# Performance work log

Measured on AMD Instinct MI355X. Metric: run time of the kernel, lower is better.

## Reference

```python
import jax, jax.numpy as jnp
import numpy as np

B, R, C = 2, 64, 256
PH = PW = 7
KMAX = 8            # max pool-kernel size per axis given roi size bounds (kernel<=7 here)
HW = [160, 80, 40, 20]   # FPN level spatial sizes for a 640px image, strides 4/8/16/32
STRIDES = [4.0, 8.0, 16.0, 32.0]
TOP = 224.0         # config.top_pyramid_roi_size
HIDDEN = 2048
NCLS = 20
SCALE = float(np.round(np.sqrt(C), 2))  # np.round(sqrt(inner_dim),2) in SelfAttention


def setup_inputs() -> dict:
    key = jax.random.key(0)
    ks = jax.random.split(key, 32)
    U = lambda k, s, lo, hi: jax.random.uniform(k, s, minval=lo, maxval=hi)
    x1 = U(ks[0], (B, R), 0.0, 260.0)
    y1 = U(ks[1], (B, R), 0.0, 260.0)
    w = U(ks[2], (B, R), 16.0, 360.0)
    h = U(ks[3], (B, R), 16.0, 360.0)
    rois = jnp.stack([x1, y1, jnp.minimum(x1 + w, 639.0), jnp.minimum(y1 + h, 639.0)], -1)
    N = lambda k, s, sc: (sc * jax.random.normal(k, s)).astype(jnp.float32)
    inp = {'rois': rois}
    for i in range(4):
        inp[f'fm{i}'] = N(ks[4 + i], (B, C, HW[i], HW[i]), 1.0)
    inp['wq'] = N(ks[8], (C, C), 0.02);  inp['bq'] = jnp.zeros((C,), jnp.float32)
    inp['wk'] = N(ks[9], (C, C), 0.02);  inp['bk'] = jnp.zeros((C,), jnp.float32)
    inp['wv'] = N(ks[10], (C, C), 0.02); inp['bv'] = jnp.zeros((C,), jnp.float32)
    inp['wo'] = N(ks[11], (C, C), 0.02); inp['bo'] = jnp.zeros((C,), jnp.float32)
    inp['w1'] = N(ks[12], (C * PH * PW, HIDDEN), 0.02); inp['b1'] = jnp.zeros((HIDDEN,), jnp.float32)
    inp['w2'] = N(ks[13], (HIDDEN, HIDDEN), 0.02);       inp['b2'] = jnp.zeros((HIDDEN,), jnp.float32)
    inp['wreg'] = N(ks[14], (HIDDEN, 4 * (NCLS + 1)), 0.02); inp['breg'] = jnp.zeros((4 * (NCLS + 1),), jnp.float32)
    inp['wcls'] = N(ks[15], (HIDDEN, NCLS + 1), 0.02);       inp['bcls'] = jnp.zeros((NCLS + 1,), jnp.float32)
    return inp


def _forward(rois, fm0, fm1, fm2, fm3, wq, bq, wk, bk, wv, bv, wo, bo,
             w1, b1, w2, b2, wreg, breg, wcls, bcls):
    Hmax = HW[0]
    pad = lambda fm: jnp.pad(fm, ((0, 0), (0, 0), (0, Hmax - fm.shape[-2]), (0, Hmax - fm.shape[-1])))
    feats = jnp.stack([pad(fm0), pad(fm1), pad(fm2), pad(fm3)])  # [4,B,C,Hmax,Hmax]
    heights = jnp.array(HW, jnp.int32)
    strides = jnp.array(STRIDES, jnp.float32)

    r = rois.reshape(-1, 4)                 # [N,4] xyxy in pixels
    Nroi = r.shape[0]
    bidx = jnp.repeat(jnp.arange(B, dtype=jnp.int32), R)
    size = jnp.sqrt((r[:, 2] - r[:, 0]) * (r[:, 3] - r[:, 1]))
    # int() truncates toward zero, then clamp(0,3) -- matches torch
    lvl = jnp.clip((3.0 + jnp.log(size / TOP)).astype(jnp.int32), 0, 3)
    s = strides[lvl]
    x1 = (r[:, 0] / s).astype(jnp.int32); y1 = (r[:, 1] / s).astype(jnp.int32)
    x2 = (r[:, 2] / s).astype(jnp.int32); y2 = (r[:, 3] / s).astype(jnp.int32)
    Hl = heights[lvl]                        # per-roi level map size (square maps)

    def expand(lo, hi, cap, pool):
        # replicate the symmetric while-loop expansion until span >= pool
        for _ in range(pool):
            need = (hi - lo + 1) < pool
            lo = jnp.where(need, jnp.maximum(lo - 1, 0), lo)
            hi = jnp.where(need, jnp.minimum(hi + 1, cap - 1), hi)
        return lo, hi

    y1, y2 = expand(y1, y2, Hl, PH)
    x1, x2 = expand(x1, x2, Hl, PW)
    rh = y2 - y1 + 1; rw = x2 - x1 + 1
    kh = (rh + PH - 1) // PH; sh = rh // PH   # ceil / floor kernel & stride
    kw = (rw + PW - 1) // PW; sw = rw // PW

    ar_p = jnp.arange(PH); ar_k = jnp.arange(KMAX)

    def pool_one(l, b, yy, xx, kh_, kw_, sh_, sw_):
        rows = jnp.clip(yy + ar_p[:, None] * sh_ + ar_k[None, :], 0, Hmax - 1)  # [PH,K]
        cols = jnp.clip(xx + ar_p[:, None] * sw_ + ar_k[None, :], 0, Hmax - 1)  # [PW,K]
        patch = feats[l, b][:, rows[:, :, None, None], cols[None, None, :, :]]  # [C,PH,K,PW,K]
        m = (ar_k < kh_)[:, None, None] & (ar_k < kw_)[None, None, :]           # [K,1,K] -> bcast
        patch = jnp.where(m, patch, -jnp.inf)
        return patch.max(axis=(2, 4))                                           # [C,PH,PW]

    pooled = jax.vmap(pool_one)(lvl, bidx, y1, x1, kh, kw, sh, sw)  # [N,C,PH,PW]

    # SelfAttention over the PH*PW spatial tokens of each ROI
    L = PH * PW
    tok = pooled.reshape(Nroi, C, L).transpose(0, 2, 1)            # [N,L,C]
    q = tok @ wq + bq
    k = tok @ wk + bk
    v = tok @ wv + bv
    att = jax.nn.softmax(jnp.einsum('nlc,nmc->nlm', q, k) / SCALE, axis=-1)
    ctx = jnp.einsum('nlm,nmc->nlc', att, v) @ wo + bo             # [N,L,C]
    x = pooled.reshape(Nroi, C, L) + ctx.transpose(0, 2, 1)        # residual add
    x = x.reshape(Nroi, C * L)

    h1 = jax.nn.relu(x @ w1 + b1)
    h2 = jax.nn.relu(h1 @ w2 + b2)
    bbox_reg = h2 @ wreg + breg                                    # [N, 4*(NCLS+1)]
    bbox_classes = jax.nn.softmax(h2 @ wcls + bcls, axis=-1)       # [N, NCLS+1]
    return bbox_reg, bbox_classes


def reference(rois, fm0, fm1, fm2, fm3, wq, bq, wk, bk, wv, bv, wo, bo,
              w1, b1, w2, b2, wreg, breg, wcls, bcls):
    return _forward(rois, fm0, fm1, fm2, fm3, wq, bq, wk, bk, wv, bv, wo, bo,
                    w1, b1, w2, b2, wreg, breg, wcls, bcls)
```

## Files before the change

kernel.cpp:

```cpp
#include <hip/hip_runtime.h>
#include <hip/hip_bf16.h>
#include <stdint.h>

typedef __attribute__((ext_vector_type(8))) short bf16x8;
typedef __attribute__((ext_vector_type(4))) float f32x4;

__device__ __forceinline__ float blo(unsigned u){ union{float f;unsigned x;}v; v.x = u<<16; return v.f; }
__device__ __forceinline__ float bhi(unsigned u){ union{float f;unsigned x;}v; v.x = u & 0xFFFF0000u; return v.f; }
__device__ __forceinline__ unsigned short f2bf(float f){
  union{float f;unsigned x;}v; v.f=f; unsigned x=v.x;
  return (unsigned short)((x + 0x7fffu + ((x>>16)&1u)) >> 16);
}
__device__ __forceinline__ unsigned cvtpk(float lo, float hi){
  unsigned r;
  asm("v_cvt_pk_bf16_f32 %0, %1, %2" : "=v"(r) : "v"(lo), "v"(hi));
  return r;
}

__global__ __launch_bounds__(256) void pool_pack_kernel(
    const float* __restrict__ rois,
    const float* __restrict__ fm0, const float* __restrict__ fm1,
    const float* __restrict__ fm2, const float* __restrict__ fm3,
    float* __restrict__ pooled, unsigned short* __restrict__ tok,
    const float* __restrict__ wreg, const float* __restrict__ wcls, float* __restrict__ wT)
{
  int bx = blockIdx.x;
  int tid = threadIdx.x;
  if (bx >= 896){
    int c = bx - 896;
    if (c < 84){
      for (int k = tid; k < 2048; k += 256) wT[(size_t)c*2048 + k] = wreg[(size_t)k*84 + c];
    } else {
      int cc = c - 84;
      for (int k = tid; k < 2048; k += 256) wT[(size_t)c*2048 + k] = wcls[(size_t)k*21 + cc];
    }
    return;
  }
  int n = bx / 7;
  int ph = bx - n*7;
  int c = tid;
  const float* r = rois + n*4;
  int b = n >> 6;
  float rx1=r[0], ry1=r[1], rx2=r[2], ry2=r[3];
  float size = sqrtf((rx2-rx1)*(ry2-ry1));
  int lvl = (int)(3.0f + logf(size/224.0f));
  if (lvl < 0) lvl = 0; if (lvl > 3) lvl = 3;
  const float strides_[4] = {4.f,8.f,16.f,32.f};
  const int hw_[4] = {160,80,40,20};
  float s = strides_[lvl]; int Hl = hw_[lvl];
  int x1 = (int)(rx1/s), y1 = (int)(ry1/s), x2 = (int)(rx2/s), y2 = (int)(ry2/s);
  #pragma unroll
  for (int it=0; it<7; ++it){
    bool need = (y2-y1+1) < 7;
    if (need){ y1 = (y1-1 > 0) ? y1-1 : 0; y2 = (y2+1 < Hl-1) ? y2+1 : Hl-1; }
  }
  #pragma unroll
  for (int it=0; it<7; ++it){
    bool need = (x2-x1+1) < 7;
    if (need){ x1 = (x1-1 > 0) ? x1-1 : 0; x2 = (x2+1 < Hl-1) ? x2+1 : Hl-1; }
  }
  int rh = y2-y1+1, rw = x2-x1+1;
  int kh = (rh+6)/7, sh = rh/7, kw = (rw+6)/7, sw2 = rw/7;
  const float* fm = (lvl==0)?fm0:(lvl==1)?fm1:(lvl==2)?fm2:fm3;
  const float* fp = fm + ((size_t)(b*256 + c))*(size_t)(Hl*Hl);
  int r0 = y1 + ph*sh;
  for (int pw=0; pw<7; ++pw){
    int c0 = x1 + pw*sw2;
    float m = -3.4e38f;
    for (int i=0;i<kh;++i){
      const float* rp = fp + (size_t)(r0+i)*Hl + c0;
      for (int j=0;j<kw;++j) m = fmaxf(m, rp[j]);
    }
    int l = ph*7+pw;
    pooled[((size_t)n*256 + c)*49 + l] = m;
    tok[((size_t)n*49 + l)*256 + c] = f2bf(m);
  }
}

template<int EPI, bool XCDR>
__global__ __launch_bounds__(256) void gemm_kernel(
    const unsigned short* __restrict__ A,
    const float* __restrict__ B0, const float* __restrict__ B1, const float* __restrict__ B2,
    const float* __restrict__ bias0, const float* __restrict__ bias1, const float* __restrict__ bias2,
    unsigned short* __restrict__ o0, unsigned short* __restrict__ o1, unsigned short* __restrict__ o2,
    float* __restrict__ outf, const float* __restrict__ pooled,
    int M, int Nper, int K, int nM, int nN, int kChunk)
{
  __shared__ __align__(16) unsigned short Bs[2][2048];
  int bid = blockIdx.x;
  if constexpr (XCDR){
    int pe = gridDim.x >> 3;
    bid = (bid & 7)*pe + (bid >> 3);
  }
  int per = nM*nN;
  int kc  = bid / per;
  int rem = bid - kc*per;
  int bm = rem % nM, bn = rem / nM;
  int m0 = bm*64, n0 = bn*64;
  int mat = n0 / Nper;
  int col0 = n0 - mat*Nper;
  const float* Bp    = (mat==0)?B0:(mat==1)?B1:B2;
  const float* biasp = (mat==0)?bias0:(mat==1)?bias1:bias2;
  unsigned short* outp = (mat==0)?o0:(mat==1)?o1:o2;
  int k0 = kc*kChunk;
  int nMacro = kChunk >> 7;
  int tid = threadIdx.x, lane = tid & 63, wave = tid >> 6;
  int wm = wave & 1, wn = wave >> 1;
  int g = lane >> 4, c = lane & 15;

  f32x4 acc[2][2];
  #pragma unroll
  for (int i=0;i<2;++i)
    #pragma unroll
    for (int j=0;j<2;++j){ acc[i][j][0]=0.f; acc[i][j][1]=0.f; acc[i][j][2]=0.f; acc[i][j][3]=0.f; }

  int brow = tid >> 3, bcg = tid & 7;
  int bw_idx = brow*64 + ((bcg*8) ^ ((brow>>3)<<4));
  const float* Bbase = Bp + (size_t)brow*Nper + col0 + bcg*8;
  int rb0 = g*512 + (((wn*2  )^g)*16 + c);
  int rb1 = g*512 + (((wn*2+1)^g)*16 + c);
  const unsigned short* Ap0 = A + (size_t)(m0 + wm*32 +      c)*K + g*8;
  const unsigned short* Ap1 = A + (size_t)(m0 + wm*32 + 16 + c)*K + g*8;

  auto writeB = [&](int buf, const float4& bx, const float4& by){
    uint4 w;
    w.x = cvtpk(bx.x,bx.y); w.y = cvtpk(bx.z,bx.w);
    w.z = cvtpk(by.x,by.y); w.w = cvtpk(by.z,by.w);
    *(uint4*)&Bs[buf][bw_idx] = w;
  };
  auto readFrags = [&](int buf, bf16x8& r0, bf16x8& r1){
    union { unsigned short s[8]; bf16x8 v; } u0, u1;
    const unsigned short* bsp = &Bs[buf][0];
    #pragma unroll
    for (int j=0;j<8;++j){ u0.s[j] = bsp[rb0 + j*64]; u1.s[j] = bsp[rb1 + j*64]; }
    r0 = u0.v; r1 = u1.v;
  };
  auto mfma4 = [&](const bf16x8& f0, const bf16x8& f1, const bf16x8& q0, const bf16x8& q1){
    acc[0][0] = __builtin_amdgcn_mfma_f32_16x16x32_bf16(f0,q0,acc[0][0],0,0,0);
    acc[0][1] = __builtin_amdgcn_mfma_f32_16x16x32_bf16(f0,q1,acc[0][1],0,0,0);
    acc[1][0] = __builtin_amdgcn_mfma_f32_16x16x32_bf16(f1,q0,acc[1][0],0,0,0);
    acc[1][1] = __builtin_amdgcn_mfma_f32_16x16x32_bf16(f1,q1,acc[1][1],0,0,0);
  };

  for (int mi = 0; mi < nMacro; ++mi){
    int kk = k0 + (mi << 7);
    uint4 a0x = *(const uint4*)(Ap0+kk),    a0y = *(const uint4*)(Ap1+kk);
    uint4 a1x = *(const uint4*)(Ap0+kk+32), a1y = *(const uint4*)(Ap1+kk+32);
    uint4 a2x = *(const uint4*)(Ap0+kk+64), a2y = *(const uint4*)(Ap1+kk+64);
    uint4 a3x = *(const uint4*)(Ap0+kk+96), a3y = *(const uint4*)(Ap1+kk+96);
    const float* p0 = Bbase + (size_t)kk*Nper;
    const float* p1 = p0 + (size_t)32*Nper;
    const float* p2 = p0 + (size_t)64*Nper;
    const float* p3 = p0 + (size_t)96*Nper;
    float4 b0a = *(const float4*)p0, b0b = *(const float4*)(p0+4);
    float4 b1a = *(const float4*)p1, b1b = *(const float4*)(p1+4);
    float4 b2a = *(const float4*)p2, b2b = *(const float4*)(p2+4);
    float4 b3a = *(const float4*)p3, b3b = *(const float4*)(p3+4);

    writeB(0, b0a, b0b);
    __syncthreads();

    bf16x8 q0,q1;
    readFrags(0,q0,q1);
    writeB(1,b1a,b1b);
    mfma4(*(const bf16x8*)&a0x, *(const bf16x8*)&a0y, q0,q1);
    __syncthreads();

    readFrags(1,q0,q1);
    writeB(0,b2a,b2b);
    mfma4(*(const bf16x8*)&a1x, *(const bf16x8*)&a1y, q0,q1);
    __syncthreads();

    readFrags(0,q0,q1);
    writeB(1,b3a,b3b);
    mfma4(*(const bf16x8*)&a2x, *(const bf16x8*)&a2y, q0,q1);
    __syncthreads();

    readFrags(1,q0,q1);
    mfma4(*(const bf16x8*)&a3x, *(const bf16x8*)&a3y, q0,q1);
  }

  int rq = g << 2, cl = c;
  #pragma unroll
  for (int mr=0;mr<2;++mr){
    #pragma unroll
    for (int nc=0;nc<2;++nc){
      int rowb = m0 + wm*32 + mr*16 + rq;
      int colM = col0 + wn*32 + nc*16 + cl;
      #pragma unroll
      for (int r2=0;r2<4;++r2){
        float v = acc[mr][nc][r2];
        int rr = rowb + r2;
        if constexpr (EPI==0){
          v += biasp[colM];
          outp[(size_t)rr*Nper + colM] = f2bf(v);
        } else if constexpr (EPI==1){
          v += biasp[colM];
          int nn = rr/49, l = rr - nn*49;
          v += pooled[((size_t)nn*256 + colM)*49 + l];
          outp[(size_t)nn*12544 + colM*49 + l] = f2bf(v);
        } else {
          outf[(size_t)kc*M*Nper + (size_t)rr*Nper + colM] = v;
        }
      }
    }
  }
}

__global__ __launch_bounds__(256) void reduce1_kernel(
    const float* __restrict__ part, const float* __restrict__ b1,
    unsigned short* __restrict__ h1, int nPart)
{
  int i = blockIdx.x*256 + threadIdx.x;
  float4 s = ((const float4*)part)[i];
  for (int kc = 1; kc < nPart; ++kc){
    float4 p = ((const float4*)part)[(size_t)kc*65536 + i];
    s.x += p.x; s.y += p.y; s.z += p.z; s.w += p.w;
  }
  float4 bb = *(const float4*)(b1 + ((i<<2) & 2047));
  s.x = fmaxf(s.x+bb.x,0.f); s.y = fmaxf(s.y+bb.y,0.f);
  s.z = fmaxf(s.z+bb.z,0.f); s.w = fmaxf(s.w+bb.w,0.f);
  uint2 w;
  w.x = cvtpk(s.x, s.y); w.y = cvtpk(s.z, s.w);
  *(uint2*)&h1[(size_t)i<<2] = w;
}

__global__ __launch_bounds__(256) void reduce2_kernel(
    const float* __restrict__ part, float* __restrict__ h2f, int nPart)
{
  int i = blockIdx.x*256 + threadIdx.x;
  float4 s = ((const float4*)part)[i];
  for (int kc = 1; kc < nPart; ++kc){
    float4 p = ((const float4*)part)[(size_t)kc*65536 + i];
    s.x += p.x; s.y += p.y; s.z += p.z; s.w += p.w;
  }
  ((float4*)h2f)[i] = s;
}

__global__ __launch_bounds__(256) void attn_kernel(
    const unsigned short* __restrict__ Q, const unsigned short* __restrict__ Km,
    const unsigned short* __restrict__ V, unsigned short* __restrict__ ctx)
{
  int n = blockIdx.x, half = blockIdx.y, tid = threadIdx.x;
  int r0 = half*25, rcnt = half ? 24 : 25;
  __shared__ __align__(16) unsigned short qs[25*256];
  __shared__ __align__(16) unsigned short ks[49*260];
  __shared__ float S[25*49];
  const uint4* qg = (const uint4*)(Q + ((size_t)n*49 + r0)*256);
  for (int i = tid; i < rcnt*32; i += 256) ((uint4*)qs)[i] = qg[i];
  const uint2* kg = (const uint2*)(Km + (size_t)n*49*256);
  for (int i = tid; i < 49*64; i += 256){
    int j = i >> 6, s = i & 63;
    *(uint2*)(ks + j*260 + s*4) = kg[i];
  }
  __syncthreads();
  for (int p = tid; p < rcnt*49; p += 256){
    int i = p/49, j = p - i*49;
    const uint2* qr = (const uint2*)(qs + i*256);
    const uint2* kr = (const uint2*)(ks + j*260);
    float sum = 0.f;
    #pragma unroll 8
    for (int c4 = 0; c4 < 64; ++c4){
      uint2 qv = qr[c4], kv = kr[c4];
      sum += blo(qv.x)*blo(kv.x) + bhi(qv.x)*bhi(kv.x);
      sum += blo(qv.y)*blo(kv.y) + bhi(qv.y)*bhi(kv.y);
    }
    S[p] = sum * (1.0f/16.0f);
  }
  __syncthreads();
  const uint2* vg = (const uint2*)(V + (size_t)n*49*256);
  for (int i = tid; i < 49*64; i += 256){
    int j = i >> 6, s = i & 63;
    *(uint2*)(ks + j*260 + s*4) = vg[i];
  }
  if (tid < rcnt){
    float* row = S + tid*49;
    float mx = row[0];
    for (int j=1;j<49;++j) mx = fmaxf(mx,row[j]);
    float sm = 0.f;
    for (int j=0;j<49;++j){ float e = expf(row[j]-mx); row[j]=e; sm+=e; }
    float inv = 1.0f/sm;
    for (int j=0;j<49;++j) row[j] *= inv;
  }
  __syncthreads();
  for (int idx = tid; idx < rcnt*64; idx += 256){
    int i = idx >> 6, cp4 = idx & 63;
    const float* att = S + i*49;
    float s0=0.f, s1=0.f, s2=0.f, s3=0.f;
    #pragma unroll 7
    for (int j=0;j<49;++j){
      uint2 v = *(const uint2*)(ks + j*260 + cp4*4);
      float a = att[j];
      s0 += a*blo(v.x); s1 += a*bhi(v.x);
      s2 += a*blo(v.y); s3 += a*bhi(v.y);
    }
    uint2 outw;
    outw.x = (unsigned)f2bf(s0) | ((unsigned)f2bf(s1) << 16);
    outw.y = (unsigned)f2bf(s2) | ((unsigned)f2bf(s3) << 16);
    *(uint2*)&ctx[((size_t)n*49 + r0 + i)*256 + cp4*4] = outw;
  }
}

__global__ __launch_bounds__(256) void heads_dot(
    const float* __restrict__ h2f, const float* __restrict__ b2,
    const float* __restrict__ wT,
    const float* __restrict__ breg, const float* __restrict__ bcls,
    float* __restrict__ out, float* __restrict__ logits)
{
  int gw = (blockIdx.x*256 + threadIdx.x) >> 6;
  int lane = threadIdx.x & 63;
  int m = gw / 105, c = gw - m*105;
  const float4* hp = (const float4*)(h2f + (size_t)m*2048);
  const float4* bp = (const float4*)b2;
  const float4* wp = (const float4*)(wT + (size_t)c*2048);
  float sum = 0.f;
  #pragma unroll
  for (int i=0;i<8;++i){
    float4 a = hp[i*64 + lane];
    float4 bb = bp[i*64 + lane];
    float4 w = wp[i*64 + lane];
    sum += fmaxf(a.x+bb.x,0.f)*w.x + fmaxf(a.y+bb.y,0.f)*w.y
         + fmaxf(a.z+bb.z,0.f)*w.z + fmaxf(a.w+bb.w,0.f)*w.w;
  }
  #pragma unroll
  for (int off=32; off; off>>=1) sum += __shfl_down(sum, off, 64);
  if (lane == 0){
    if (c < 84) out[(size_t)m*84 + c] = sum + breg[c];
    else        logits[(size_t)m*21 + (c-84)] = sum + bcls[c-84];
  }
}

__global__ __launch_bounds__(128) void cls_softmax(
    const float* __restrict__ logits, float* __restrict__ out)
{
  int m = threadIdx.x;
  const float* lg = logits + (size_t)m*21;
  float mx = lg[0];
  #pragma unroll
  for (int j=1;j<21;++j) mx = fmaxf(mx, lg[j]);
  float sm = 0.f;
  float e[21];
  #pragma unroll
  for (int j=0;j<21;++j){ e[j] = expf(lg[j]-mx); sm += e[j]; }
  float inv = 1.0f/sm;
  #pragma unroll
  for (int j=0;j<21;++j) out[10752 + (size_t)m*21 + j] = e[j]*inv;
}

extern "C" void kernel_launch(void* const* d_in, const int* in_sizes, int n_in,
                              void* d_out, int out_size, void* d_ws, size_t ws_size,
                              hipStream_t stream)
{
  (void)in_sizes; (void)n_in; (void)out_size; (void)ws_size;
  const float* rois = (const float*)d_in[0];
  const float* fm0  = (const float*)d_in[1];
  const float* fm1  = (const float*)d_in[2];
  const float* fm2  = (const float*)d_in[3];
  const float* fm3  = (const float*)d_in[4];
  const float* wq   = (const float*)d_in[5];
  const float* bq   = (const float*)d_in[6];
  const float* wk   = (const float*)d_in[7];
  const float* bk   = (const float*)d_in[8];
  const float* wv   = (const float*)d_in[9];
  const float* bv   = (const float*)d_in[10];
  const float* wo   = (const float*)d_in[11];
  const float* bo   = (const float*)d_in[12];
  const float* w1   = (const float*)d_in[13];
  const float* b1   = (const float*)d_in[14];
  const float* w2   = (const float*)d_in[15];
  const float* b2   = (const float*)d_in[16];
  const float* wreg = (const float*)d_in[17];
  const float* breg = (const float*)d_in[18];
  const float* wcls = (const float*)d_in[19];
  const float* bcls = (const float*)d_in[20];
  float* out = (float*)d_out;

  char* ws = (char*)d_ws;
  float*          pooled = (float*)(ws + 0);
  unsigned short* tok    = (unsigned short*)(ws + 6422528);
  unsigned short* Qb     = (unsigned short*)(ws + 9633792);
  unsigned short* Kb     = (unsigned short*)(ws + 12845056);
  unsigned short* Vb     = (unsigned short*)(ws + 16056320);
  unsigned short* ctx    = (unsigned short*)(ws + 19267584);
  unsigned short* xb     = (unsigned short*)(ws + 22478848);
  float*          h2f    = (float*)(ws + 25690112);
  unsigned short* h1     = (unsigned short*)(ws + 26738688);
  float*          wT     = (float*)(ws + 27787264);
  float*          logits = (float*)(ws + 28647424);
  float*          h1part = (float*)(ws + 0);
  float*          h2part = (float*)(ws + 0);

  pool_pack_kernel<<<1001,256,0,stream>>>(rois, fm0, fm1, fm2, fm3, pooled, tok,
                                          wreg, wcls, wT);

  gemm_kernel<0,false><<<1176,256,0,stream>>>(tok, wq,wk,wv, bq,bk,bv,
                                              Qb,Kb,Vb, nullptr, nullptr,
                                              6272,256,256, 98,12, 256);

  attn_kernel<<<dim3(128,2),256,0,stream>>>(Qb, Kb, Vb, ctx);

  gemm_kernel<1,false><<<392,256,0,stream>>>(ctx, wo,wo,wo, bo,bo,bo,
                                             xb,xb,xb, nullptr, pooled,
                                             6272,256,256, 98,4, 256);

  gemm_kernel<2,true><<<896,256,0,stream>>>(xb, w1,w1,w1, nullptr,nullptr,nullptr,
                                            nullptr,nullptr,nullptr, h1part, nullptr,
                                            128,2048,12544, 2,32, 896);
  reduce1_kernel<<<256,256,0,stream>>>(h1part, b1, h1, 14);

  gemm_kernel<2,true><<<1024,256,0,stream>>>(h1, w2,w2,w2, nullptr,nullptr,nullptr,
                                             nullptr,nullptr,nullptr, h2part, nullptr,
                                             128,2048,2048, 2,32, 128);
  reduce2_kernel<<<256,256,0,stream>>>(h2part, h2f, 16);

  heads_dot<<<3360,256,0,stream>>>(h2f, b2, wT, breg, bcls, out, logits);
  cls_softmax<<<1,128,0,stream>>>(logits, out);
}
```

Measured before the change: 187.9 us.

## Stage fp32 weight tiles into LDS via direct global-to-LDS loads

The GEMM's B (weight) operand is now copied straight from global memory into an fp32 LDS double buffer with global_load_lds, rather than loaded into registers, converted to bf16 and written to LDS. Conversion to bf16 happens after the LDS read, just before the MFMAs. The loop now steps 32 k-values per iteration with a prefetch of the next tile, replacing the 128-wide macro step. The aim is to cut register pressure and VGPR-to-LDS store traffic. In exchange it doubles LDS footprint, adds conversion work on every fragment read, and puts a barrier on every 32-k step, losing the multi-step register prefetch of A and B.

```diff
diff --git a/kernel.cpp b/kernel.cpp
--- a/kernel.cpp
+++ b/kernel.cpp
@@ -15,6 +15,11 @@
   unsigned r;
   asm("v_cvt_pk_bf16_f32 %0, %1, %2" : "=v"(r) : "v"(lo), "v"(hi));
   return r;
+}
+__device__ __forceinline__ void gll16(const float* g, float* l){
+  __builtin_amdgcn_global_load_lds(
+      (const __attribute__((address_space(1))) unsigned int*)g,
+      (__attribute__((address_space(3))) unsigned int*)l, 16, 0, 0);
 }
 
 __global__ __launch_bounds__(256) void pool_pack_kernel(
@@ -86,7 +91,7 @@
     float* __restrict__ outf, const float* __restrict__ pooled,
     int M, int Nper, int K, int nM, int nN, int kChunk)
 {
-  __shared__ __align__(16) unsigned short Bs[2][2048];
+  __shared__ __align__(16) float Bs[2][32][64];
   int bid = blockIdx.x;
   if constexpr (XCDR){
     int pe = gridDim.x >> 3;
@@ -102,8 +107,7 @@
   const float* Bp    = (mat==0)?B0:(mat==1)?B1:B2;
   const float* biasp = (mat==0)?bias0:(mat==1)?bias1:bias2;
   unsigned short* outp = (mat==0)?o0:(mat==1)?o1:o2;
-  int k0 = kc*kChunk;
-  int nMacro = kChunk >> 7;
+  int k0 = kc*kChunk, k1 = k0 + kChunk;
   int tid = threadIdx.x, lane = tid & 63, wave = tid >> 6;
   int wm = wave & 1, wn = wave >> 1;
   int g = lane >> 4, c = lane & 15;
@@ -114,70 +118,38 @@
     #pragma unroll
     for (int j=0;j<2;++j){ acc[i][j][0]=0.f; acc[i][j][1]=0.f; acc[i][j][2]=0.f; acc[i][j][3]=0.f; }
 
-  int brow = tid >> 3, bcg = tid & 7;
-  int bw_idx = brow*64 + ((bcg*8) ^ ((brow>>3)<<4));
-  const float* Bbase = Bp + (size_t)brow*Nper + col0 + bcg*8;
-  int rb0 = g*512 + (((wn*2  )^g)*16 + c);
-  int rb1 = g*512 + (((wn*2+1)^g)*16 + c);
+  const float* Bg = Bp + (size_t)(wave*8 + (lane>>4))*Nper + col0 + (lane&15)*4;
   const unsigned short* Ap0 = A + (size_t)(m0 + wm*32 +      c)*K + g*8;
   const unsigned short* Ap1 = A + (size_t)(m0 + wm*32 + 16 + c)*K + g*8;
 
-  auto writeB = [&](int buf, const float4& bx, const float4& by){
-    uint4 w;
-    w.x = cvtpk(bx.x,bx.y); w.y = cvtpk(bx.z,bx.w);
-    w.z = cvtpk(by.x,by.y); w.w = cvtpk(by.z,by.w);
-    *(uint4*)&Bs[buf][bw_idx] = w;
+  auto stage = [&](int buf, int kk){
+    gll16(Bg + (size_t)kk*Nper,     &Bs[buf][wave*8    ][0]);
+    gll16(Bg + (size_t)(kk+4)*Nper, &Bs[buf][wave*8 + 4][0]);
   };
-  auto readFrags = [&](int buf, bf16x8& r0, bf16x8& r1){
-    union { unsigned short s[8]; bf16x8 v; } u0, u1;
-    const unsigned short* bsp = &Bs[buf][0];
+
+  stage(0, k0);
+  int buf = 0;
+  for (int kk = k0; kk < k1; kk += 32){
+    __syncthreads();
+    if (kk + 32 < k1) stage(buf^1, kk+32);
+    uint4 a0 = *(const uint4*)(Ap0 + kk);
+    uint4 a1 = *(const uint4*)(Ap1 + kk);
+    const float* fb = &Bs[buf][g*8][wn*32 + c];
+    float q0f[8], q1f[8];
     #pragma unroll
-    for (int j=0;j<8;++j){ u0.s[j] = bsp[rb0 + j*64]; u1.s[j] = bsp[rb1 + j*64]; }
-    r0 = u0.v; r1 = u1.v;
-  };
-  auto mfma4 = [&](const bf16x8& f0, const bf16x8& f1, const bf16x8& q0, const bf16x8& q1){
-    acc[0][0] = __builtin_amdgcn_mfma_f32_16x16x32_bf16(f0,q0,acc[0][0],0,0,0);
-    acc[0][1] = __builtin_amdgcn_mfma_f32_16x16x32_bf16(f0,q1,acc[0][1],0,0,0);
-    acc[1][0] = __builtin_amdgcn_mfma_f32_16x16x32_bf16(f1,q0,acc[1][0],0,0,0);
-    acc[1][1] = __builtin_amdgcn_mfma_f32_16x16x32_bf16(f1,q1,acc[1][1],0,0,0);
-  };
-
-  for (int mi = 0; mi < nMacro; ++mi){
-    int kk = k0 + (mi << 7);
-    uint4 a0x = *(const uint4*)(Ap0+kk),    a0y = *(const uint4*)(Ap1+kk);
-    uint4 a1x = *(const uint4*)(Ap0+kk+32), a1y = *(const uint4*)(Ap1+kk+32);
-    uint4 a2x = *(const uint4*)(Ap0+kk+64), a2y = *(const uint4*)(Ap1+kk+64);
-    uint4 a3x = *(const uint4*)(Ap0+kk+96), a3y = *(const uint4*)(Ap1+kk+96);
-    const float* p0 = Bbase + (size_t)kk*Nper;
-    const float* p1 = p0 + (size_t)32*Nper;
-    const float* p2 = p0 + (size_t)64*Nper;
-    const float* p3 = p0 + (size_t)96*Nper;
-    float4 b0a = *(const float4*)p0, b0b = *(const float4*)(p0+4);
-    float4 b1a = *(const float4*)p1, b1b = *(const float4*)(p1+4);
-    float4 b2a = *(const float4*)p2, b2b = *(const float4*)(p2+4);
-    float4 b3a = *(const float4*)p3, b3b = *(const float4*)(p3+4);
-
-    writeB(0, b0a, b0b);
-    __syncthreads();
-
-    bf16x8 q0,q1;
-    readFrags(0,q0,q1);
-    writeB(1,b1a,b1b);
-    mfma4(*(const bf16x8*)&a0x, *(const bf16x8*)&a0y, q0,q1);
-    __syncthreads();
-
-    readFrags(1,q0,q1);
-    writeB(0,b2a,b2b);
-    mfma4(*(const bf16x8*)&a1x, *(const bf16x8*)&a1y, q0,q1);
-    __syncthreads();
-
-    readFrags(0,q0,q1);
-    writeB(1,b3a,b3b);
-    mfma4(*(const bf16x8*)&a2x, *(const bf16x8*)&a2y, q0,q1);
-    __syncthreads();
-
-    readFrags(1,q0,q1);
-    mfma4(*(const bf16x8*)&a3x, *(const bf16x8*)&a3y, q0,q1);
+    for (int j=0;j<8;++j){ q0f[j] = fb[j*64]; q1f[j] = fb[j*64 + 16]; }
+    union { unsigned u[4]; bf16x8 v; } q0u, q1u;
+    q0u.u[0]=cvtpk(q0f[0],q0f[1]); q0u.u[1]=cvtpk(q0f[2],q0f[3]);
+    q0u.u[2]=cvtpk(q0f[4],q0f[5]); q0u.u[3]=cvtpk(q0f[6],q0f[7]);
+    q1u.u[0]=cvtpk(q1f[0],q1f[1]); q1u.u[1]=cvtpk(q1f[2],q1f[3]);
+    q1u.u[2]=cvtpk(q1f[4],q1f[5]); q1u.u[3]=cvtpk(q1f[6],q1f[7]);
+    bf16x8 f0 = *(const bf16x8*)&a0;
+    bf16x8 f1 = *(const bf16x8*)&a1;
+    acc[0][0] = __builtin_amdgcn_mfma_f32_16x16x32_bf16(f0,q0u.v,acc[0][0],0,0,0);
+    acc[0][1] = __builtin_amdgcn_mfma_f32_16x16x32_bf16(f0,q1u.v,acc[0][1],0,0,0);
+    acc[1][0] = __builtin_amdgcn_mfma_f32_16x16x32_bf16(f1,q0u.v,acc[1][0],0,0,0);
+    acc[1][1] = __builtin_amdgcn_mfma_f32_16x16x32_bf16(f1,q1u.v,acc[1][1],0,0,0);
+    buf ^= 1;
   }
 
   int rq = g << 2, cl = c;
```

Result: no change. 184.8 us (-1.6%).

## Add LDS-async fc kernel with gathered w1 rows and token-major pooled layout

Applied to the files above, without the earlier changes.

Replaces the generic split-K GEMM for the two big FC layers with a dedicated fc_kernel. It streams fp32 weight rows into LDS through global_load_lds with a 4-deep buffer ring and explicit vmcnt waits, then converts to bf16 at fragment read. The activation x is now stored token-major (l*256+c), and w1 rows are gathered with a permuted index so the math still matches the channel-major flatten. The pooled buffer also moves to token-major to simplify the residual epilogue. The w1 GEMM is split into more K chunks (28 instead of 14), which raises parallelism at the cost of a larger partial-sum reduction.

```diff
diff --git a/kernel.cpp b/kernel.cpp
--- a/kernel.cpp
+++ b/kernel.cpp
@@ -15,6 +15,11 @@
   unsigned r;
   asm("v_cvt_pk_bf16_f32 %0, %1, %2" : "=v"(r) : "v"(lo), "v"(hi));
   return r;
+}
+__device__ __forceinline__ void gll16(const float* g, float* l){
+  __builtin_amdgcn_global_load_lds(
+      (const __attribute__((address_space(1))) unsigned int*)g,
+      (__attribute__((address_space(3))) unsigned int*)l, 16, 0, 0);
 }
 
 __global__ __launch_bounds__(256) void pool_pack_kernel(
@@ -72,26 +77,117 @@
       for (int j=0;j<kw;++j) m = fmaxf(m, rp[j]);
     }
     int l = ph*7+pw;
-    pooled[((size_t)n*256 + c)*49 + l] = m;
+    pooled[((size_t)n*49 + l)*256 + c] = m;
     tok[((size_t)n*49 + l)*256 + c] = f2bf(m);
   }
 }
 
-template<int EPI, bool XCDR>
+template<bool GATHER>
+__global__ __launch_bounds__(256) void fc_kernel(
+    const unsigned short* __restrict__ A, const float* __restrict__ B,
+    float* __restrict__ outf, int M, int K, int kChunk)
+{
+  __shared__ __align__(16) float Bs[4][32][64];
+  int bid = blockIdx.x;
+  int pe = gridDim.x >> 3;
+  bid = (bid & 7)*pe + (bid >> 3);
+  const int per = 64;
+  int kc = bid / per;
+  int rem = bid - kc*per;
+  int bm = rem & 1, bn = rem >> 1;
+  int m0 = bm*64, n0 = bn*64;
+  int tid = threadIdx.x, lane = tid & 63, wave = tid >> 6;
+  int wm = wave & 1, wn = wave >> 1;
+  int g = lane >> 4, c = lane & 15;
+  int k0 = kc*kChunk;
+  int nSteps = kChunk >> 5;
+
+  f32x4 acc[2][2];
+  #pragma unroll
+  for (int i=0;i<2;++i)
+    #pragma unroll
+    for (int j=0;j<2;++j){ acc[i][j][0]=0.f; acc[i][j][1]=0.f; acc[i][j][2]=0.f; acc[i][j][3]=0.f; }
+
+  int rowInWave = lane >> 4;
+  int colOff = n0 + (lane & 15)*4;
+  const unsigned short* Ap0 = A + (size_t)(m0 + wm*32 +      c)*K + g*8;
+  const unsigned short* Ap1 = A + (size_t)(m0 + wm*32 + 16 + c)*K + g*8;
+
+  auto srcRow = [&](int k)->const float*{
+    if constexpr (GATHER){ int kk = k; return B + ((size_t)((kk & 255)*49 + (kk >> 8)))*2048; }
+    else                 { return B + (size_t)k*2048; }
+  };
+  auto stage = [&](int buf, int kk){
+    int r0a = kk + wave*8 + rowInWave;
+    int r0b = r0a + 4;
+    gll16(srcRow(r0a) + colOff, &Bs[buf][wave*8    ][0]);
+    gll16(srcRow(r0b) + colOff, &Bs[buf][wave*8 + 4][0]);
+  };
+
+  stage(0, k0); stage(1, k0+32); stage(2, k0+64);
+  uint4 aCur0 = *(const uint4*)(Ap0 + k0);
+  uint4 aCur1 = *(const uint4*)(Ap1 + k0);
+
+  for (int i = 0; i < nSteps; ++i){
+    int kk = k0 + (i<<5);
+    int pend = nSteps - i;
+    if (pend >= 3)      asm volatile("s_waitcnt vmcnt(4)" ::: "memory");
+    else if (pend == 2) asm volatile("s_waitcnt vmcnt(2)" ::: "memory");
+    else                asm volatile("s_waitcnt vmcnt(0)" ::: "memory");
+    __builtin_amdgcn_s_barrier();
+
+    uint4 aNxt0 = aCur0, aNxt1 = aCur1;
+    if (i+1 < nSteps){
+      aNxt0 = *(const uint4*)(Ap0 + kk + 32);
+      aNxt1 = *(const uint4*)(Ap1 + kk + 32);
+    }
+    if (i+3 < nSteps) stage((i+3)&3, kk + 96);
+
+    const float* fb = &Bs[i&3][g*8][wn*32 + c];
+    float q0f[8], q1f[8];
+    #pragma unroll
+    for (int j=0;j<8;++j){ q0f[j] = fb[j*64]; q1f[j] = fb[j*64 + 16]; }
+    union { unsigned u[4]; bf16x8 v; } q0u, q1u;
+    q0u.u[0]=cvtpk(q0f[0],q0f[1]); q0u.u[1]=cvtpk(q0f[2],q0f[3]);
+    q0u.u[2]=cvtpk(q0f[4],q0f[5]); q0u.u[3]=cvtpk(q0f[6],q0f[7]);
+    q1u.u[0]=cvtpk(q1f[0],q1f[1]); q1u.u[1]=cvtpk(q1f[2],q1f[3]);
+    q1u.u[2]=cvtpk(q1f[4],q1f[5]); q1u.u[3]=cvtpk(q1f[6],q1f[7]);
+    bf16x8 f0 = *(const bf16x8*)&aCur0;
+    bf16x8 f1 = *(const bf16x8*)&aCur1;
+    acc[0][0] = __builtin_amdgcn_mfma_f32_16x16x32_bf16(f0,q0u.v,acc[0][0],0,0,0);
+    acc[0][1] = __builtin_amdgcn_mfma_f32_16x16x32_bf16(f0,q1u.v,acc[0][1],0,0,0);
+    acc[1][0] = __builtin_amdgcn_mfma_f32_16x16x32_bf16(f1,q0u.v,acc[1][0],0,0,0);
+    acc[1][1] = __builtin_amdgcn_mfma_f32_16x16x32_bf16(f1,q1u.v,acc[1][1],0,0,0);
+    aCur0 = aNxt0; aCur1 = aNxt1;
+  }
+
+  int rq = g << 2;
+  #pragma unroll
+  for (int mr=0;mr<2;++mr){
+    #pragma unroll
+    for (int nc=0;nc<2;++nc){
+      int rowb = m0 + wm*32 + mr*16 + rq;
+      int colM = n0 + wn*32 + nc*16 + c;
+      #pragma unroll
+      for (int r2=0;r2<4;++r2){
+        outf[(size_t)kc*M*2048 + (size_t)(rowb+r2)*2048 + colM] = acc[mr][nc][r2];
+      }
+    }
+  }
+}
+
+template<int EPI>
 __global__ __launch_bounds__(256) void gemm_kernel(
     const unsigned short* __restrict__ A,
     const float* __restrict__ B0, const float* __restrict__ B1, const float* __restrict__ B2,
     const float* __restrict__ bias0, const float* __restrict__ bias1, const float* __restrict__ bias2,
     unsigned short* __restrict__ o0, unsigned short* __restrict__ o1, unsigned short* __restrict__ o2,
-    float* __restrict__ outf, const float* __restrict__ pooled,
+    const float* __restrict__ pooled,
     int M, int Nper, int K, int nM, int nN, int kChunk)
 {
   __shared__ __align__(16) unsigned short Bs[2][2048];
   int bid = blockIdx.x;
-  if constexpr (XCDR){
-    int pe = gridDim.x >> 3;
-    bid = (bid & 7)*pe + (bid >> 3);
-  }
+  int tid = threadIdx.x;
   int per = nM*nN;
   int kc  = bid / per;
   int rem = bid - kc*per;
@@ -104,7 +200,7 @@
   unsigned short* outp = (mat==0)?o0:(mat==1)?o1:o2;
   int k0 = kc*kChunk;
   int nMacro = kChunk >> 7;
-  int tid = threadIdx.x, lane = tid & 63, wave = tid >> 6;
+  int lane = tid & 63, wave = tid >> 6;
   int wm = wave & 1, wn = wave >> 1;
   int g = lane >> 4, c = lane & 15;
 
@@ -159,23 +255,19 @@
 
     writeB(0, b0a, b0b);
     __syncthreads();
-
     bf16x8 q0,q1;
     readFrags(0,q0,q1);
     writeB(1,b1a,b1b);
     mfma4(*(const bf16x8*)&a0x, *(const bf16x8*)&a0y, q0,q1);
     __syncthreads();
-
     readFrags(1,q0,q1);
     writeB(0,b2a,b2b);
     mfma4(*(const bf16x8*)&a1x, *(const bf16x8*)&a1y, q0,q1);
     __syncthreads();
-
     readFrags(0,q0,q1);
     writeB(1,b3a,b3b);
     mfma4(*(const bf16x8*)&a2x, *(const bf16x8*)&a2y, q0,q1);
     __syncthreads();
-
     readFrags(1,q0,q1);
     mfma4(*(const bf16x8*)&a3x, *(const bf16x8*)&a3y, q0,q1);
   }
@@ -194,13 +286,11 @@
         if constexpr (EPI==0){
           v += biasp[colM];
           outp[(size_t)rr*Nper + colM] = f2bf(v);
-        } else if constexpr (EPI==1){
+        } else {
           v += biasp[colM];
+          v += pooled[(size_t)rr*256 + colM];
           int nn = rr/49, l = rr - nn*49;
-          v += pooled[((size_t)nn*256 + colM)*49 + l];
-          outp[(size_t)nn*12544 + colM*49 + l] = f2bf(v);
-        } else {
-          outf[(size_t)kc*M*Nper + (size_t)rr*Nper + colM] = v;
+          outp[(size_t)nn*12544 + l*256 + colM] = f2bf(v);
         }
       }
     }
@@ -387,30 +477,26 @@
   unsigned short* h1     = (unsigned short*)(ws + 26738688);
   float*          wT     = (float*)(ws + 27787264);
   float*          logits = (float*)(ws + 28647424);
-  float*          h1part = (float*)(ws + 0);
-  float*          h2part = (float*)(ws + 0);
+  float*          h1part = (float*)(ws + 29360128);
+  float*          h2part = (float*)(ws + 29360128);
 
   pool_pack_kernel<<<1001,256,0,stream>>>(rois, fm0, fm1, fm2, fm3, pooled, tok,
                                           wreg, wcls, wT);
 
-  gemm_kernel<0,false><<<1176,256,0,stream>>>(tok, wq,wk,wv, bq,bk,bv,
-                                              Qb,Kb,Vb, nullptr, nullptr,
-                                              6272,256,256, 98,12, 256);
+  gemm_kernel<0><<<1176,256,0,stream>>>(tok, wq,wk,wv, bq,bk,bv,
+                                        Qb,Kb,Vb, nullptr,
+                                        6272,256,256, 98,12, 256);
 
   attn_kernel<<<dim3(128,2),256,0,stream>>>(Qb, Kb, Vb, ctx);
 
-  gemm_kernel<1,false><<<392,256,0,stream>>>(ctx, wo,wo,wo, bo,bo,bo,
-                                             xb,xb,xb, nullptr, pooled,
-                                             6272,256,256, 98,4, 256);
-
-  gemm_kernel<2,true><<<896,256,0,stream>>>(xb, w1,w1,w1, nullptr,nullptr,nullptr,
-                                            nullptr,nullptr,nullptr, h1part, nullptr,
-                                            128,2048,12544, 2,32, 896);
-  reduce1_kernel<<<256,256,0,stream>>>(h1part, b1, h1, 14);
-
-  gemm_kernel<2,true><<<1024,256,0,stream>>>(h1, w2,w2,w2, nullptr,nullptr,nullptr,
-                                             nullptr,nullptr,nullptr, h2part, nullptr,
-                                             128,2048,2048, 2,32, 128);
+  gemm_kernel<1><<<392,256,0,stream>>>(ctx, wo,wo,wo, bo,bo,bo,
+                                       xb,xb,xb, pooled,
+                                       6272,256,256, 98,4, 256);
+
+  fc_kernel<true><<<1792,256,0,stream>>>(xb, w1, h1part, 128, 12544, 448);
+  reduce1_kernel<<<256,256,0,stream>>>(h1part, b1, h1, 28);
+
+  fc_kernel<false><<<1024,256,0,stream>>>(h1, w2, h2part, 128, 2048, 128);
   reduce2_kernel<<<256,256,0,stream>>>(h2part, h2f, 16);
 
   heads_dot<<<3360,256,0,stream>>>(h2f, b2, wT, breg, bcls, out, logits);
```

Result: faster. 161.6 us (-14.0%).
